# Optimization experiments

Hardware: AMD Instinct MI355X
Metric: run time of the kernel (lower is better)

The kernel has to match this reference:

```python
import jax, jax.numpy as jnp
import numpy as np

IMG = 224      # image_size
P = 16         # patch_size
HP = P // 2    # half_patch
D = 768        # projection_dim
C_IN = 3
B = 64


def setup_inputs() -> dict:
    key = jax.random.key(0)
    k1, k2 = jax.random.split(key, 2)
    images = jax.random.normal(k1, (B, IMG, IMG, C_IN), dtype=jnp.float32)
    pvs = P * P * C_IN * 5  # patch_vector_size with 5-way channel concat
    W = jax.random.normal(k2, (pvs, D), dtype=jnp.float32) * 0.02
    b = jnp.zeros((D,), dtype=jnp.float32)
    return {"images": images, "W": W, "b": b}


def _crop_shift_pad(images, oh, ow):
    # Faithful to the TF code: crop at (oh, ow) then pad back at the SAME
    # (oh, ow) -> identity inside the region, zeros on the complementary border.
    th = IMG - HP
    tw = IMG - HP
    out = jnp.zeros_like(images)
    return out.at[:, oh:oh + th, ow:ow + tw, :].set(images[:, oh:oh + th, ow:ow + tw, :])


def reference(images, W, b):
    # 4 shifted-pad variants: left-up, left-down, right-up, right-down
    offsets = [(0, 0), (HP, 0), (0, HP), (HP, HP)]
    concat = jnp.concatenate(
        [images] + [_crop_shift_pad(images, oh, ow) for oh, ow in offsets],
        axis=-1)  # (B, IMG, IMG, 5*C_IN)
    Bn, _, _, C = concat.shape
    g = IMG // P  # grid size = 14
    # tf.image.extract_patches with stride==size, VALID: non-overlapping patches,
    # patch contents row-major with channel fastest -> reshape/transpose.
    x = concat.reshape(Bn, g, P, g, P, C)
    x = x.transpose(0, 1, 3, 2, 4, 5).reshape(Bn, g * g, P * P * C)  # (B, 196, 3840)
    return x @ W + b  # (B, 196, 768)
```

## Files before the change

kernel.cpp:

```cpp
#include <hip/hip_runtime.h>
#include <hip/hip_bf16.h>

typedef _Float16 half8 __attribute__((ext_vector_type(8)));
typedef _Float16 half4 __attribute__((ext_vector_type(4)));
typedef float floatx4 __attribute__((ext_vector_type(4)));

#define PD 768
#define KE 768
#define NB 64

__device__ __forceinline__ int cls_row_base(int cls) {
  return (cls == 0) ? 0 : (cls == 1) ? 64 : (cls == 2) ? 832 : (cls == 3) ? 896
       : (cls == 4) ? 1664 : (cls == 5) ? 10880 : (cls == 6) ? 11648
       : (cls == 7) ? 11712 : 12480;
}

__device__ __forceinline__ void gl_lds16(const _Float16* g, _Float16* l) {
  __builtin_amdgcn_global_load_lds(
      (const __attribute__((address_space(1))) unsigned int*)g,
      (__attribute__((address_space(3))) unsigned int*)l, 16, 0, 0);
}

__global__ __launch_bounds__(256) void prep_weights(
    const float* __restrict__ W, _Float16* __restrict__ Weff) {
  __shared__ float Wl[240][68];
  const int t  = threadIdx.x;
  const int ck = blockIdx.x & 15;
  const int cd = blockIdx.x >> 4;
  const int p0 = ck * 16;
  const int d0 = cd * 64;
#pragma unroll
  for (int i = 0; i < 15; ++i) {
    int c = i * 256 + t;
    int row = c >> 4, off = (c & 15) * 4;
    *(floatx4*)&Wl[row][off] =
        *(const floatx4*)&W[(size_t)(p0 * 15 + row) * PD + d0 + off];
  }
  __syncthreads();
#pragma unroll
  for (int i = 0; i < 3; ++i) {
    int wi = i * 256 + t;
    int d = wi / 12, q = wi - d * 12;
    float vout[9][4];
#pragma unroll
    for (int s = 0; s < 4; ++s) {
      int kl = q * 4 + s;
      int pl = kl / 3, cc = kl - pl * 3;
      int pix = p0 + pl;
      int ph = pix >> 4, pw = pix & 15;
      int rb = pl * 15 + cc;
      float w0 = Wl[rb][d],     w1 = Wl[rb + 3][d], w2 = Wl[rb + 6][d],
            w3 = Wl[rb + 9][d], w4 = Wl[rb + 12][d];
      float hlt[3] = {1.f, 1.f, (ph < 8) ? 1.f : 0.f};
      float hge[3] = {(ph >= 8) ? 1.f : 0.f, 1.f, 1.f};
      float wlt[3] = {1.f, 1.f, (pw < 8) ? 1.f : 0.f};
      float wge[3] = {(pw >= 8) ? 1.f : 0.f, 1.f, 1.f};
#pragma unroll
      for (int rh = 0; rh < 3; ++rh)
#pragma unroll
        for (int rw = 0; rw < 3; ++rw)
          vout[rh * 3 + rw][s] = w0 + hlt[rh] * wlt[rw] * w1
              + hge[rh] * wlt[rw] * w2 + hlt[rh] * wge[rw] * w3
              + hge[rh] * wge[rw] * w4;
    }
#pragma unroll
    for (int cls = 0; cls < 9; ++cls) {
      half4 h;
      h.x = (_Float16)vout[cls][0]; h.y = (_Float16)vout[cls][1];
      h.z = (_Float16)vout[cls][2]; h.w = (_Float16)vout[cls][3];
      *(half4*)&Weff[((size_t)cls * PD + d0 + d) * KE + ck * 48 + q * 4] = h;
    }
  }
}

__global__ __launch_bounds__(256) void prep_imcol(
    const float* __restrict__ img, _Float16* __restrict__ Ap) {
  const int total = NB * 224 * 84;
  for (int id = blockIdx.x * 256 + threadIdx.x; id < total; id += 2048 * 256) {
    int b   = id / 18816;
    int rem = id - b * 18816;
    int h   = rem / 84;
    int c8  = rem - h * 84;
    int gw  = c8 / 6;
    int j8  = c8 - gw * 6;
    int gh  = h >> 4, ph = h & 15;
    int rh  = (gh == 0) ? 0 : ((gh >= 13) ? 2 : 1);
    int rw  = (gw == 0) ? 0 : ((gw >= 13) ? 2 : 1);
    int gh0 = (rh == 1) ? 1 : ((rh == 2) ? 13 : 0);
    int gw0 = (rw == 1) ? 1 : ((rw == 2) ? 13 : 0);
    int nh  = (rh == 1) ? 12 : 1;
    int nw  = (rw == 1) ? 12 : 1;
    int cls = rh * 3 + rw;
    int r   = cls_row_base(cls) + (b * nh + (gh - gh0)) * nw + (gw - gw0);
    const float* src = img + (size_t)(b * 224 + h) * 672 + c8 * 8;
    floatx4 v0 = *(const floatx4*)src;
    floatx4 v1 = *(const floatx4*)(src + 4);
    half8 o;
    o[0] = (_Float16)v0.x; o[1] = (_Float16)v0.y;
    o[2] = (_Float16)v0.z; o[3] = (_Float16)v0.w;
    o[4] = (_Float16)v1.x; o[5] = (_Float16)v1.y;
    o[6] = (_Float16)v1.z; o[7] = (_Float16)v1.w;
    *(half8*)&Ap[(size_t)r * KE + ph * 48 + j8 * 8] = o;
  }
}

__global__ __launch_bounds__(256) void spt_gemm(
    const _Float16* __restrict__ Ap, const _Float16* __restrict__ Weff,
    const float* __restrict__ bias, float* __restrict__ out) {
  __shared__ _Float16 Al[2][64 * 64];
  __shared__ _Float16 Bl[2][128 * 64];

  const int t  = threadIdx.x;
  const int nt = blockIdx.x % 6;
  const int bt = blockIdx.x / 6;

  int cls;
  if      (bt < 1)   cls = 0;
  else if (bt < 13)  cls = 1;
  else if (bt < 14)  cls = 2;
  else if (bt < 26)  cls = 3;
  else if (bt < 170) cls = 4;
  else if (bt < 182) cls = 5;
  else if (bt < 183) cls = 6;
  else if (bt < 195) cls = 7;
  else               cls = 8;

  const int w = t >> 6, lane = t & 63;
  const int wr = w >> 1, wc = w & 1;
  const int lrow = lane & 15, lq = lane >> 4;

  const int srow = t >> 3;
  const int js = (t & 7) ^ (srow & 7);
  const _Float16* Ag = Ap + (size_t)(bt * 64 + srow) * KE + js * 8;
  const _Float16* Bg = Weff + ((size_t)cls * PD + nt * 128 + srow) * KE + js * 8;

  floatx4 acc[2][4];
#pragma unroll
  for (int m = 0; m < 2; ++m)
#pragma unroll
    for (int n = 0; n < 4; ++n) acc[m][n] = (floatx4)0.f;

#define STAGE(ks, sel)                                                        \
  {                                                                           \
    _Pragma("unroll")                                                         \
    for (int i = 0; i < 2; ++i)                                               \
      gl_lds16(Ag + (size_t)i * 32 * KE + (ks) * 64,                          \
               &Al[sel][i * 2048 + w * 512]);                                 \
    _Pragma("unroll")                                                         \
    for (int i = 0; i < 4; ++i)                                               \
      gl_lds16(Bg + (size_t)i * 32 * KE + (ks) * 64,                          \
               &Bl[sel][i * 2048 + w * 512]);                                 \
  }

  int cur = 0;
  STAGE(0, 0);
  __syncthreads();
  for (int ks = 0; ks < 12; ++ks) {
    if (ks < 11) STAGE(ks + 1, cur ^ 1);
#pragma unroll
    for (int kf = 0; kf < 2; ++kf) {
      half8 af[2], bf[4];
#pragma unroll
      for (int m = 0; m < 2; ++m) {
        int row = wr * 32 + m * 16 + lrow;
        af[m] = *(const half8*)&Al[cur][row * 64
                 + ((kf * 32 + lq * 8) ^ ((row & 7) * 8))];
      }
#pragma unroll
      for (int n = 0; n < 4; ++n) {
        int row = wc * 64 + n * 16 + lrow;
        bf[n] = *(const half8*)&Bl[cur][row * 64
                 + ((kf * 32 + lq * 8) ^ ((row & 7) * 8))];
      }
#pragma unroll
      for (int m = 0; m < 2; ++m)
#pragma unroll
        for (int n = 0; n < 4; ++n)
          acc[m][n] = __builtin_amdgcn_mfma_f32_16x16x32_f16(
              af[m], bf[n], acc[m][n], 0, 0, 0);
    }
    __syncthreads();
    cur ^= 1;
  }

  const int rh  = cls / 3, rw = cls % 3;
  const int gh0 = (rh == 1) ? 1 : ((rh == 2) ? 13 : 0);
  const int gw0 = (rw == 1) ? 1 : ((rw == 2) ? 13 : 0);
  const int nw  = (rw == 1) ? 12 : 1;
  const int nh  = (rh == 1) ? 12 : 1;
  const int per = nh * nw;
  const int cbase = cls_row_base(cls);

  const int col = nt * 128 + wc * 64 + lrow;
  float bv[4];
#pragma unroll
  for (int n = 0; n < 4; ++n) bv[n] = bias[col + n * 16];
  const int rq = lq * 4;
#pragma unroll
  for (int m = 0; m < 2; ++m) {
#pragma unroll
    for (int j = 0; j < 4; ++j) {
      int R = bt * 64 + wr * 32 + m * 16 + rq + j;
      int r = R - cbase;
      int b, ih, iw;
      if (per == 1)        { b = r; ih = 0; iw = 0; }
      else if (per == 12)  { b = r / 12; int rm = r - b * 12;
                             ih = (nw == 1) ? rm : 0; iw = (nw == 1) ? 0 : rm; }
      else                 { b = r / 144; int rm = r - b * 144;
                             ih = rm / 12; iw = rm - ih * 12; }
      int p = (gh0 + ih) * 14 + (gw0 + iw);
      float* orow = out + ((size_t)b * 196 + p) * PD + col;
#pragma unroll
      for (int n = 0; n < 4; ++n) orow[n * 16] = acc[m][n][j] + bv[n];
    }
  }
}

extern "C" void kernel_launch(void* const* d_in, const int* in_sizes, int n_in,
                              void* d_out, int out_size, void* d_ws, size_t ws_size,
                              hipStream_t stream) {
  const float* img  = (const float*)d_in[0];
  const float* W    = (const float*)d_in[1];
  const float* bias = (const float*)d_in[2];
  float* out = (float*)d_out;
  _Float16* Weff = (_Float16*)d_ws;
  _Float16* Ap   = (_Float16*)((char*)d_ws + 10616832);

  prep_weights<<<192, 256, 0, stream>>>(W, Weff);
  prep_imcol<<<2048, 256, 0, stream>>>(img, Ap);
  spt_gemm<<<196 * 6, 256, 0, stream>>>(Ap, Weff, bias, out);
}
```

Measured before the change: 137.1 us.

## Enlarge GEMM M-tile to 128 per class and split weight prep finer

The GEMM block tile grows from 64x128 to 128x128, with per-class tile indexing, clamped A-row loads and masked stores for partial tiles. This halves B-operand reloads per output and doubles MFMA work per LDS stage, at the cost of more registers and LDS, wasted work on padded rows for small classes, and fewer blocks (600 vs 1176). Separately, prep_weights is split into 768 smaller blocks with less shared memory each, to raise parallelism in the weight-folding kernel.

```diff
diff --git a/kernel.cpp b/kernel.cpp
--- a/kernel.cpp
+++ b/kernel.cpp
@@ -23,24 +23,20 @@
 
 __global__ __launch_bounds__(256) void prep_weights(
     const float* __restrict__ W, _Float16* __restrict__ Weff) {
-  __shared__ float Wl[240][68];
+  __shared__ float Wl[60][68];
   const int t  = threadIdx.x;
-  const int ck = blockIdx.x & 15;
-  const int cd = blockIdx.x >> 4;
-  const int p0 = ck * 16;
+  const int ck = blockIdx.x & 63;
+  const int cd = blockIdx.x >> 6;
+  const int p0 = ck * 4;
   const int d0 = cd * 64;
-#pragma unroll
-  for (int i = 0; i < 15; ++i) {
-    int c = i * 256 + t;
+  for (int c = t; c < 960; c += 256) {
     int row = c >> 4, off = (c & 15) * 4;
     *(floatx4*)&Wl[row][off] =
         *(const floatx4*)&W[(size_t)(p0 * 15 + row) * PD + d0 + off];
   }
   __syncthreads();
-#pragma unroll
-  for (int i = 0; i < 3; ++i) {
-    int wi = i * 256 + t;
-    int d = wi / 12, q = wi - d * 12;
+  if (t < 192) {
+    int d = t / 3, q = t - (t / 3) * 3;
     float vout[9][4];
 #pragma unroll
     for (int s = 0; s < 4; ++s) {
@@ -68,7 +64,7 @@
       half4 h;
       h.x = (_Float16)vout[cls][0]; h.y = (_Float16)vout[cls][1];
       h.z = (_Float16)vout[cls][2]; h.w = (_Float16)vout[cls][3];
-      *(half4*)&Weff[((size_t)cls * PD + d0 + d) * KE + ck * 48 + q * 4] = h;
+      *(half4*)&Weff[((size_t)cls * PD + d0 + d) * KE + ck * 12 + q * 4] = h;
     }
   }
 }
@@ -104,26 +100,35 @@
   }
 }
 
+#define BM 128
+#define BN 128
+
 __global__ __launch_bounds__(256) void spt_gemm(
     const _Float16* __restrict__ Ap, const _Float16* __restrict__ Weff,
     const float* __restrict__ bias, float* __restrict__ out) {
-  __shared__ _Float16 Al[2][64 * 64];
-  __shared__ _Float16 Bl[2][128 * 64];
+  __shared__ _Float16 Al[2][BM * 64];
+  __shared__ _Float16 Bl[2][BN * 64];
 
   const int t  = threadIdx.x;
   const int nt = blockIdx.x % 6;
   const int bt = blockIdx.x / 6;
 
-  int cls;
-  if      (bt < 1)   cls = 0;
-  else if (bt < 13)  cls = 1;
-  else if (bt < 14)  cls = 2;
-  else if (bt < 26)  cls = 3;
-  else if (bt < 170) cls = 4;
-  else if (bt < 182) cls = 5;
-  else if (bt < 183) cls = 6;
-  else if (bt < 195) cls = 7;
-  else               cls = 8;
+  int cls, mt;
+  if      (bt < 1)  { cls = 0; mt = bt; }
+  else if (bt < 7)  { cls = 1; mt = bt - 1; }
+  else if (bt < 8)  { cls = 2; mt = bt - 7; }
+  else if (bt < 14) { cls = 3; mt = bt - 8; }
+  else if (bt < 86) { cls = 4; mt = bt - 14; }
+  else if (bt < 92) { cls = 5; mt = bt - 86; }
+  else if (bt < 93) { cls = 6; mt = bt - 92; }
+  else if (bt < 99) { cls = 7; mt = bt - 93; }
+  else              { cls = 8; mt = bt - 99; }
+
+  const int rh  = cls / 3, rw = cls % 3;
+  const int per = ((rh == 1) ? 12 : 1) * ((rw == 1) ? 12 : 1);
+  const int Mc  = NB * per;
+  const int cbase   = cls_row_base(cls);
+  const int rowbase = cbase + mt * BM;
 
   const int w = t >> 6, lane = t & 63;
   const int wr = w >> 1, wc = w & 1;
@@ -131,25 +136,31 @@
 
   const int srow = t >> 3;
   const int js = (t & 7) ^ (srow & 7);
-  const _Float16* Ag = Ap + (size_t)(bt * 64 + srow) * KE + js * 8;
-  const _Float16* Bg = Weff + ((size_t)cls * PD + nt * 128 + srow) * KE + js * 8;
-
-  floatx4 acc[2][4];
-#pragma unroll
-  for (int m = 0; m < 2; ++m)
+  const _Float16* Agp[4];
+  const _Float16* Bgp[4];
+#pragma unroll
+  for (int i = 0; i < 4; ++i) {
+    int rA = rowbase + i * 32 + srow;
+    int rmax = cbase + Mc - 1;
+    rA = (rA > rmax) ? rmax : rA;
+    Agp[i] = Ap + (size_t)rA * KE + js * 8;
+    Bgp[i] = Weff + ((size_t)cls * PD + nt * BN + i * 32 + srow) * KE + js * 8;
+  }
+
+  floatx4 acc[4][4];
+#pragma unroll
+  for (int m = 0; m < 4; ++m)
 #pragma unroll
     for (int n = 0; n < 4; ++n) acc[m][n] = (floatx4)0.f;
 
 #define STAGE(ks, sel)                                                        \
   {                                                                           \
     _Pragma("unroll")                                                         \
-    for (int i = 0; i < 2; ++i)                                               \
-      gl_lds16(Ag + (size_t)i * 32 * KE + (ks) * 64,                          \
-               &Al[sel][i * 2048 + w * 512]);                                 \
+    for (int i = 0; i < 4; ++i)                                               \
+      gl_lds16(Agp[i] + (ks) * 64, &Al[sel][i * 2048 + w * 512]);             \
     _Pragma("unroll")                                                         \
     for (int i = 0; i < 4; ++i)                                               \
-      gl_lds16(Bg + (size_t)i * 32 * KE + (ks) * 64,                          \
-               &Bl[sel][i * 2048 + w * 512]);                                 \
+      gl_lds16(Bgp[i] + (ks) * 64, &Bl[sel][i * 2048 + w * 512]);             \
   }
 
   int cur = 0;
@@ -159,10 +170,10 @@
     if (ks < 11) STAGE(ks + 1, cur ^ 1);
 #pragma unroll
     for (int kf = 0; kf < 2; ++kf) {
-      half8 af[2], bf[4];
-#pragma unroll
-      for (int m = 0; m < 2; ++m) {
-        int row = wr * 32 + m * 16 + lrow;
+      half8 af[4], bf[4];
+#pragma unroll
+      for (int m = 0; m < 4; ++m) {
+        int row = wr * 64 + m * 16 + lrow;
         af[m] = *(const half8*)&Al[cur][row * 64
                  + ((kf * 32 + lq * 8) ^ ((row & 7) * 8))];
       }
@@ -173,7 +184,7 @@
                  + ((kf * 32 + lq * 8) ^ ((row & 7) * 8))];
       }
 #pragma unroll
-      for (int m = 0; m < 2; ++m)
+      for (int m = 0; m < 4; ++m)
 #pragma unroll
         for (int n = 0; n < 4; ++n)
           acc[m][n] = __builtin_amdgcn_mfma_f32_16x16x32_f16(
@@ -183,35 +194,33 @@
     cur ^= 1;
   }
 
-  const int rh  = cls / 3, rw = cls % 3;
   const int gh0 = (rh == 1) ? 1 : ((rh == 2) ? 13 : 0);
   const int gw0 = (rw == 1) ? 1 : ((rw == 2) ? 13 : 0);
   const int nw  = (rw == 1) ? 12 : 1;
-  const int nh  = (rh == 1) ? 12 : 1;
-  const int per = nh * nw;
-  const int cbase = cls_row_base(cls);
-
-  const int col = nt * 128 + wc * 64 + lrow;
+
+  const int col = nt * BN + wc * 64 + lrow;
   float bv[4];
 #pragma unroll
   for (int n = 0; n < 4; ++n) bv[n] = bias[col + n * 16];
   const int rq = lq * 4;
 #pragma unroll
-  for (int m = 0; m < 2; ++m) {
+  for (int m = 0; m < 4; ++m) {
 #pragma unroll
     for (int j = 0; j < 4; ++j) {
-      int R = bt * 64 + wr * 32 + m * 16 + rq + j;
+      int R = rowbase + wr * 64 + m * 16 + rq + j;
       int r = R - cbase;
-      int b, ih, iw;
-      if (per == 1)        { b = r; ih = 0; iw = 0; }
-      else if (per == 12)  { b = r / 12; int rm = r - b * 12;
-                             ih = (nw == 1) ? rm : 0; iw = (nw == 1) ? 0 : rm; }
-      else                 { b = r / 144; int rm = r - b * 144;
-                             ih = rm / 12; iw = rm - ih * 12; }
-      int p = (gh0 + ih) * 14 + (gw0 + iw);
-      float* orow = out + ((size_t)b * 196 + p) * PD + col;
-#pragma unroll
-      for (int n = 0; n < 4; ++n) orow[n * 16] = acc[m][n][j] + bv[n];
+      if (r < Mc) {
+        int b, ih, iw;
+        if (per == 1)        { b = r; ih = 0; iw = 0; }
+        else if (per == 12)  { b = r / 12; int rm = r - b * 12;
+                               ih = (nw == 1) ? rm : 0; iw = (nw == 1) ? 0 : rm; }
+        else                 { b = r / 144; int rm = r - b * 144;
+                               ih = rm / 12; iw = rm - ih * 12; }
+        int p = (gh0 + ih) * 14 + (gw0 + iw);
+        float* orow = out + ((size_t)b * 196 + p) * PD + col;
+#pragma unroll
+        for (int n = 0; n < 4; ++n) orow[n * 16] = acc[m][n][j] + bv[n];
+      }
     }
   }
 }
@@ -226,7 +235,7 @@
   _Float16* Weff = (_Float16*)d_ws;
   _Float16* Ap   = (_Float16*)((char*)d_ws + 10616832);
 
-  prep_weights<<<192, 256, 0, stream>>>(W, Weff);
+  prep_weights<<<768, 256, 0, stream>>>(W, Weff);
   prep_imcol<<<2048, 256, 0, stream>>>(img, Ap);
-  spt_gemm<<<196 * 6, 256, 0, stream>>>(Ap, Weff, bias, out);
-}
+  spt_gemm<<<600, 256, 0, stream>>>(Ap, Weff, bias, out);
+}
```

Result: slower. 143.0 us (+4.2%).
